# Optimization experiments

Hardware: AMD Instinct MI355X
Metric: run time of the kernel (lower is better)

## Reference

```python
import jax, jax.numpy as jnp
import numpy as np

N = 1024   # nnodes
H = 8      # attention heads
C = 32     # gnn_repr_size (per head)
HC = H * C # 256
E = 65536  # num edges
ER = 32    # edge_repr_size
F = 3      # feat_emb_size
NUM_STOPS = 512


def setup_inputs() -> dict:
    key = jax.random.key(0)
    ks = jax.random.split(key, 24)
    g = lambda i, shape, s: jax.random.normal(ks[i], shape, dtype=jnp.float32) * s
    return {
        "dist": jax.random.uniform(ks[0], (N, N), dtype=jnp.float32),
        "stops": jax.random.randint(ks[1], (NUM_STOPS,), 0, N),
        "weekday": 3,
        "vehicles": 5,
        "markov": jax.random.uniform(ks[2], (N, N), dtype=jnp.float32),
        "demand": jax.random.uniform(ks[3], (N, 1), dtype=jnp.float32),
        "capacity": 10,
        "edge_index": jax.random.randint(ks[4], (2, E), 0, N),
        # GATConv layer 1 (in=1, out=H*C, edge_dim=1)
        "W1": g(5, (1, HC), 1.0), "We1": g(6, (1, HC), 1.0),
        "a_src1": g(7, (H, C), 0.1), "a_dst1": g(8, (H, C), 0.1), "a_edge1": g(9, (H, C), 0.1),
        "b1": jnp.zeros((HC,), jnp.float32),
        # GATConv layer 2 (in=H*C, out=H*C)
        "W2": g(10, (HC, HC), 0.0625), "We2": g(11, (1, HC), 1.0),
        "a_src2": g(12, (H, C), 0.1), "a_dst2": g(13, (H, C), 0.1), "a_edge2": g(14, (H, C), 0.1),
        "b2": jnp.zeros((HC,), jnp.float32),
        # edge summarizer Linear(2*HC, ER)
        "Wes": g(15, (2 * HC, ER), 0.0442), "bes": jnp.zeros((ER,), jnp.float32),
        # scalar embeddings
        "emb_weekday": g(16, (7, F), 0.1), "emb_capacity": g(17, (26, F), 0.1), "emb_vehicle": g(18, (15, F), 0.1),
        # combiner MLP: Linear(N*ER + 3N + 3F, N), Linear(N, N)
        "Wc1": g(19, (N * ER + 3 * N + 3 * F, N), 0.0053), "bc1": jnp.zeros((N,), jnp.float32),
        "Wc2": g(20, (N, N), 0.03125), "bc2": jnp.zeros((N,), jnp.float32),
    }


def _gat(x, src, dst, edge_attr, W, We, a_src, a_dst, a_edge, b):
    """PyG GATConv (concat heads, eval mode so attention dropout is identity)."""
    h = (x @ W).reshape(-1, H, C)                   # [N, H, C]
    e = (edge_attr @ We).reshape(-1, H, C)          # [E, H, C]
    alpha = (h * a_src).sum(-1)[src] + (h * a_dst).sum(-1)[dst] + (e * a_edge).sum(-1)  # [E, H]
    alpha = jax.nn.leaky_relu(alpha, 0.2)
    # segment softmax over destination nodes
    m = jax.ops.segment_max(alpha, dst, num_segments=N)
    m = jnp.where(jnp.isfinite(m), m, 0.0)
    ex = jnp.exp(alpha - m[dst])
    denom = jax.ops.segment_sum(ex, dst, num_segments=N)
    coef = ex / (denom[dst] + 1e-16)                # [E, H]
    out = jax.ops.segment_sum(h[src] * coef[:, :, None], dst, num_segments=N)  # [N, H, C]
    return out.reshape(-1, HC) + b


def reference(dist, stops, weekday, vehicles, markov, demand, capacity, edge_index,
              W1, We1, a_src1, a_dst1, a_edge1, b1,
              W2, We2, a_src2, a_dst2, a_edge2, b2,
              Wes, bes, emb_weekday, emb_capacity, emb_vehicle,
              Wc1, bc1, Wc2, bc2):
    src, dst = edge_index[0], edge_index[1]
    dist = (dist - dist.min()) / (dist.max() - dist.min())
    edge_attr = markov[src, dst][:, None]           # [E, 1]
    x = _gat(demand, src, dst, edge_attr, W1, We1, a_src1, a_dst1, a_edge1, b1)
    x = jax.nn.relu(x)
    x = _gat(x, src, dst, edge_attr, W2, We2, a_src2, a_dst2, a_edge2, b2)
    x = jax.nn.relu(x)                              # [N, HC]
    # edge_summarizer(cat(x_i, x_j)) decomposed: x_i @ Wes_top + x_j @ Wes_bot + bes
    ea = x @ Wes[:HC]                               # [N, ER]
    eb = x @ Wes[HC:]                               # [N, ER]
    edge_repr = (ea[:, None, :] + eb[None, :, :] + bes).reshape(N, N * ER)
    wf = jnp.broadcast_to(emb_weekday[weekday][None, :], (N, F))
    cf = jnp.broadcast_to(emb_capacity[capacity][None, :], (N, F))
    vf = jnp.broadcast_to(emb_vehicle[vehicles][None, :], (N, F))
    sf = jnp.zeros((N,), jnp.float32).at[stops].set(1.0)
    sf = jnp.broadcast_to(sf[None, :], (N, N))
    combined = jnp.concatenate([edge_repr, dist, markov, wf, cf, vf, sf], axis=1)
    out = jax.nn.relu(combined @ Wc1 + bc1) @ Wc2 + bc2  # [N, N]
    return out
```

## Files before the change

### kernel.cpp

```cpp
#include <hip/hip_runtime.h>

#define NN 1024
#define NE 65536

typedef short v8s __attribute__((ext_vector_type(8)));
typedef float v4f __attribute__((ext_vector_type(4)));

constexpr size_t OF_SCAL = 0;
constexpr size_t OF_MMP  = 64;
constexpr size_t OF_DEG  = 1088;
constexpr size_t OF_OFF  = 2112;
constexpr size_t OF_CUR  = 3200;
constexpr size_t OF_EIDX = 4224;
constexpr size_t OF_MARK = 69760;
constexpr size_t OF_T1   = 135296;
constexpr size_t OF_X1   = 143488;
constexpr size_t OF_H2   = 405632;
constexpr size_t OF_S2S  = 667776;
constexpr size_t OF_S2D  = 675968;
constexpr size_t OF_MAX2 = 684160;
constexpr size_t OF_DEN2 = 692352;
constexpr size_t OF_EX2  = 700544;
constexpr size_t OF_X2   = 1224832;
constexpr size_t OF_BCAT = 1486976;
constexpr size_t OF_EAB  = 1503360;
constexpr size_t OF_WVEC = 1568896;
constexpr size_t OF_SRP  = 1604800;
constexpr size_t OF_C0P  = 3701952;
constexpr size_t OF_SR   = 3775680;
constexpr size_t OF_BASE = 3808448;
constexpr size_t OF_AH   = 3809472;
constexpr size_t OF_AL   = 4874432;
constexpr size_t OF_BTH  = 5939392;
constexpr size_t OF_BTL  = 7004352;
constexpr size_t OF_HH   = 8069312;
constexpr size_t OF_HL   = 8593600;
constexpr size_t OF_W2TH = 9117888;
constexpr size_t OF_W2TL = 9642176;
constexpr size_t OF_P0   = 10166464;

__device__ inline unsigned short f2bf(float x){
  unsigned u = __float_as_uint(x);
  unsigned r = u + 0x7fffu + ((u>>16)&1u);
  return (unsigned short)(r>>16);
}
__device__ inline float bf2f(unsigned short h){
  return __uint_as_float(((unsigned)h)<<16);
}

__global__ void k_zero(int* deg){
  int i = blockIdx.x*256 + threadIdx.x;
  if (i < NN) deg[i] = 0;
}

__global__ void k_mm1(const float* __restrict__ dist, float* mnP, float* mxP){
  __shared__ float smn[256], smx[256];
  int tid = threadIdx.x;
  float mn = 1e30f, mx = -1e30f;
  for (int i = blockIdx.x*256 + tid; i < NN*NN; i += gridDim.x*256){
    float v = dist[i]; mn = fminf(mn, v); mx = fmaxf(mx, v);
  }
  smn[tid]=mn; smx[tid]=mx; __syncthreads();
  for (int s=128; s>0; s>>=1){
    if (tid<s){ smn[tid]=fminf(smn[tid],smn[tid+s]); smx[tid]=fmaxf(smx[tid],smx[tid+s]); }
    __syncthreads();
  }
  if (tid==0){ mnP[blockIdx.x]=smn[0]; mxP[blockIdx.x]=smx[0]; }
}

__global__ void k_mm2(const float* mnP, const float* mxP, float* scal){
  __shared__ float smn[512], smx[512];
  int tid = threadIdx.x;
  smn[tid]=mnP[tid]; smx[tid]=mxP[tid]; __syncthreads();
  for (int s=256; s>0; s>>=1){
    if (tid<s){ smn[tid]=fminf(smn[tid],smn[tid+s]); smx[tid]=fmaxf(smx[tid],smx[tid+s]); }
    __syncthreads();
  }
  if (tid==0){ scal[0]=smn[0]; scal[1]=1.0f/(smx[0]-smn[0]); }
}

__global__ void k_prep(const float* W1, const float* We1, const float* as1, const float* ad1,
                       const float* ae1, const float* We2, const float* ae2, float* scal){
  int t = threadIdx.x;
  if (t < 8){
    float s=0.f, d=0.f, e=0.f, e2=0.f;
    for (int c=0;c<32;c++){
      int i = t*32+c;
      s += W1[i]*as1[i]; d += W1[i]*ad1[i]; e += We1[i]*ae1[i]; e2 += We2[i]*ae2[i];
    }
    scal[16+t]=s; scal[24+t]=d; scal[32+t]=e; scal[40+t]=e2;
  }
}

__global__ void k_edges(const int* __restrict__ ei, const float* __restrict__ markov,
                        float* __restrict__ mark, int* __restrict__ deg){
  int e = blockIdx.x*256 + threadIdx.x;
  if (e >= NE) return;
  int s = ei[e], d = ei[NE+e];
  mark[e] = markov[(size_t)s*NN + d];
  atomicAdd(&deg[d], 1);
}

__global__ void k_scan(const int* deg, int* off, int* cur){
  __shared__ int tmp[NN];
  int t = threadIdx.x;
  tmp[t] = deg[t]; __syncthreads();
  for (int s=1; s<NN; s<<=1){
    int v = (t>=s) ? tmp[t-s] : 0;
    __syncthreads();
    tmp[t] += v;
    __syncthreads();
  }
  int ex = (t==0) ? 0 : tmp[t-1];
  off[t]=ex; cur[t]=ex;
  if (t==NN-1) off[NN]=tmp[NN-1];
}

__global__ void k_fill(const int* __restrict__ ei, int* __restrict__ cur, int* __restrict__ eidxl){
  int e = blockIdx.x*256 + threadIdx.x;
  if (e >= NE) return;
  int d = ei[NE+e];
  int p = atomicAdd(&cur[d], 1);
  eidxl[p] = e;
}

__global__ __launch_bounds__(64) void k_gat1(const int* __restrict__ ei, const int* __restrict__ eidxl,
    const int* __restrict__ off, const float* __restrict__ mark, const float* __restrict__ demand,
    const float* __restrict__ scal, float* __restrict__ t1){
  int n = blockIdx.x, lane = threadIdx.x;
  int o0 = off[n], o1 = off[n+1];
  float dn = demand[n];
  float cs[8], cd[8], ce[8], mx[8];
  #pragma unroll
  for (int h=0;h<8;h++){ cs[h]=scal[16+h]; cd[h]=scal[24+h]; ce[h]=scal[32+h]; mx[h]=-1e30f; }
  for (int i=o0+lane; i<o1; i+=64){
    int e = eidxl[i]; float ds = demand[ei[e]]; float me = mark[e];
    #pragma unroll
    for (int h=0;h<8;h++){
      float a = ds*cs[h] + dn*cd[h] + me*ce[h];
      a = a < 0.f ? 0.2f*a : a;
      mx[h] = fmaxf(mx[h], a);
    }
  }
  #pragma unroll
  for (int s=32; s>0; s>>=1){
    #pragma unroll
    for (int h=0;h<8;h++) mx[h] = fmaxf(mx[h], __shfl_xor(mx[h], s));
  }
  float se[8], sd_[8];
  #pragma unroll
  for (int h=0;h<8;h++){ se[h]=0.f; sd_[h]=0.f; }
  for (int i=o0+lane; i<o1; i+=64){
    int e = eidxl[i]; float ds = demand[ei[e]]; float me = mark[e];
    #pragma unroll
    for (int h=0;h<8;h++){
      float a = ds*cs[h] + dn*cd[h] + me*ce[h];
      a = a < 0.f ? 0.2f*a : a;
      float ex = expf(a - mx[h]);
      se[h] += ex; sd_[h] += ex*ds;
    }
  }
  #pragma unroll
  for (int s=32; s>0; s>>=1){
    #pragma unroll
    for (int h=0;h<8;h++){ se[h] += __shfl_xor(se[h], s); sd_[h] += __shfl_xor(sd_[h], s); }
  }
  if (lane==0){
    #pragma unroll
    for (int h=0;h<8;h++) t1[n*8+h] = sd_[h] / (se[h] + 1e-16f);
  }
}

__global__ void k_x1(const float* __restrict__ t1, const float* __restrict__ W1,
                     const float* __restrict__ b1, float* __restrict__ x1){
  int n = blockIdx.x, hc = threadIdx.x, h = hc >> 5;
  x1[(size_t)n*256 + hc] = fmaxf(t1[n*8+h]*W1[hc] + b1[hc], 0.f);
}

__global__ __launch_bounds__(256) void gemm64(const float* __restrict__ A, int lda,
    const float* __restrict__ B, int ldb, float* __restrict__ C, int ldc, int K,
    const float* __restrict__ bias, int dorelu){
  __shared__ float As[16][68];
  __shared__ float Bs[16][68];
  int tid = threadIdx.x;
  int tx = tid & 15, ty = tid >> 4;
  int row0 = ty*4, col0 = tx*4;
  int gm = blockIdx.y*64, gn = blockIdx.x*64;
  float acc[4][4] = {};
  for (int k0 = 0; k0 < K; k0 += 16){
    #pragma unroll
    for (int q=0;q<4;q++){
      int idx = tid*4+q; int i = idx>>4, kk = idx&15;
      As[kk][i] = A[(size_t)(gm+i)*lda + k0 + kk];
    }
    #pragma unroll
    for (int q=0;q<4;q++){
      int idx = tid*4+q; int kk = idx>>6, j = idx&63;
      Bs[kk][j] = B[(size_t)(k0+kk)*ldb + gn + j];
    }
    __syncthreads();
    #pragma unroll
    for (int kk=0;kk<16;kk++){
      float a0=As[kk][row0+0], a1=As[kk][row0+1], a2=As[kk][row0+2], a3=As[kk][row0+3];
      float b0=Bs[kk][col0+0], b1=Bs[kk][col0+1], b2=Bs[kk][col0+2], b3=Bs[kk][col0+3];
      acc[0][0]+=a0*b0; acc[0][1]+=a0*b1; acc[0][2]+=a0*b2; acc[0][3]+=a0*b3;
      acc[1][0]+=a1*b0; acc[1][1]+=a1*b1; acc[1][2]+=a1*b2; acc[1][3]+=a1*b3;
      acc[2][0]+=a2*b0; acc[2][1]+=a2*b1; acc[2][2]+=a2*b2; acc[2][3]+=a2*b3;
      acc[3][0]+=a3*b0; acc[3][1]+=a3*b1; acc[3][2]+=a3*b2; acc[3][3]+=a3*b3;
    }
    __syncthreads();
  }
  #pragma unroll
  for (int i=0;i<4;i++){
    #pragma unroll
    for (int j=0;j<4;j++){
      int cc = gn + col0 + j;
      float v = acc[i][j];
      if (bias) v += bias[cc];
      if (dorelu) v = fmaxf(v, 0.f);
      C[(size_t)(gm+row0+i)*ldc + cc] = v;
    }
  }
}

__global__ void k_s2(const float* __restrict__ h2, const float* __restrict__ as2,
                     const float* __restrict__ ad2, float* __restrict__ s2s, float* __restrict__ s2d){
  int idx = blockIdx.x*256 + threadIdx.x;
  if (idx >= NN*8) return;
  int n = idx >> 3, h = idx & 7;
  float ss = 0.f, sd = 0.f;
  for (int c=0;c<32;c++){
    float v = h2[(size_t)n*256 + h*32 + c];
    ss += v*as2[h*32+c]; sd += v*ad2[h*32+c];
  }
  s2s[idx]=ss; s2d[idx]=sd;
}

__global__ __launch_bounds__(64) void k_gat2max(const int* __restrict__ ei, const int* __restrict__ eidxl,
    const int* __restrict__ off, const float* __restrict__ mark, const float* __restrict__ s2s,
    const float* __restrict__ s2d, const float* __restrict__ scal,
    float* __restrict__ mx2, float* __restrict__ den){
  int n = blockIdx.x, lane = threadIdx.x;
  int o0 = off[n], o1 = off[n+1];
  float ce[8], sdn[8], mx[8];
  #pragma unroll
  for (int h=0;h<8;h++){ ce[h]=scal[40+h]; sdn[h]=s2d[n*8+h]; mx[h]=-1e30f; }
  for (int i=o0+lane; i<o1; i+=64){
    int e = eidxl[i]; int s = ei[e]; float me = mark[e];
    #pragma unroll
    for (int h=0;h<8;h++){
      float a = s2s[s*8+h] + sdn[h] + me*ce[h];
      a = a < 0.f ? 0.2f*a : a;
      mx[h] = fmaxf(mx[h], a);
    }
  }
  #pragma unroll
  for (int sft=32; sft>0; sft>>=1){
    #pragma unroll
    for (int h=0;h<8;h++) mx[h] = fmaxf(mx[h], __shfl_xor(mx[h], sft));
  }
  float se[8];
  #pragma unroll
  for (int h=0;h<8;h++) se[h]=0.f;
  for (int i=o0+lane; i<o1; i+=64){
    int e = eidxl[i]; int s = ei[e]; float me = mark[e];
    #pragma unroll
    for (int h=0;h<8;h++){
      float a = s2s[s*8+h] + sdn[h] + me*ce[h];
      a = a < 0.f ? 0.2f*a : a;
      se[h] += expf(a - mx[h]);
    }
  }
  #pragma unroll
  for (int sft=32; sft>0; sft>>=1){
    #pragma unroll
    for (int h=0;h<8;h++) se[h] += __shfl_xor(se[h], sft);
  }
  if (lane==0){
    #pragma unroll
    for (int h=0;h<8;h++){ mx2[n*8+h] = (o1>o0) ? mx[h] : 0.f; den[n*8+h] = se[h]; }
  }
}

__global__ void k_ex2(const int* __restrict__ ei, const float* __restrict__ mark,
                      const float* __restrict__ s2s, const float* __restrict__ s2d,
                      const float* __restrict__ mx2, const float* __restrict__ scal,
                      float* __restrict__ ex2){
  int e = blockIdx.x*256 + threadIdx.x;
  if (e >= NE) return;
  int s = ei[e], d = ei[NE+e];
  float me = mark[e];
  #pragma unroll
  for (int h=0;h<8;h++){
    float a = s2s[s*8+h] + s2d[d*8+h] + me*scal[40+h];
    a = a < 0.f ? 0.2f*a : a;
    ex2[(size_t)e*8+h] = expf(a - mx2[d*8+h]);
  }
}

__global__ __launch_bounds__(256) void k_agg2(const int* __restrict__ ei, const int* __restrict__ eidxl,
    const int* __restrict__ off, const float* __restrict__ ex2, const float* __restrict__ den,
    const float* __restrict__ h2, const float* __restrict__ b2, float* __restrict__ x2){
  __shared__ int eL[64], sL[64];
  int n = blockIdx.x, tid = threadIdx.x, h = tid >> 5;
  int o0 = off[n], o1 = off[n+1];
  float inv = 1.0f/(den[n*8+h] + 1e-16f);
  float acc = 0.f;
  for (int b = o0; b < o1; b += 64){
    int len = min(64, o1 - b);
    __syncthreads();
    if (tid < len){ int e = eidxl[b+tid]; eL[tid]=e; sL[tid]=ei[e]; }
    __syncthreads();
    for (int j=0;j<len;j++){
      acc += ex2[(size_t)eL[j]*8 + h] * h2[(size_t)sL[j]*256 + tid];
    }
  }
  x2[(size_t)n*256 + tid] = fmaxf(acc*inv + b2[tid], 0.f);
}

__global__ void k_bcat(const float* __restrict__ Wes, float* __restrict__ Bcat){
  int idx = blockIdx.x*256 + threadIdx.x;
  if (idx >= 256*64) return;
  int k = idx >> 6, r = idx & 63;
  Bcat[idx] = (r < 32) ? Wes[(size_t)k*32 + r] : Wes[(size_t)(256+k)*32 + (r-32)];
}

__global__ void k_wvec(const float* __restrict__ eab, const float* __restrict__ bes,
                       const float* __restrict__ ew, const float* __restrict__ ec, const float* __restrict__ ev,
                       const int* __restrict__ wd, const int* __restrict__ cap, const int* __restrict__ veh,
                       float* __restrict__ wvec){
  int m = blockIdx.x*256 + threadIdx.x;
  if (m >= 35849) return;
  float v;
  if (m < 32768){ int j = m >> 5, r = m & 31; v = eab[(size_t)j*64 + 32 + r] + bes[r]; }
  else if (m < 34816) v = 0.f;
  else if (m < 34819) v = ew[wd[0]*3 + (m-34816)];
  else if (m < 34822) v = ec[cap[0]*3 + (m-34819)];
  else if (m < 34825) v = ev[veh[0]*3 + (m-34822)];
  else v = 0.f;
  wvec[m] = v;
}

__global__ void k_stops(const int* __restrict__ stops, float* __restrict__ wvec){
  wvec[34825 + stops[threadIdx.x]] = 1.0f;
}

__global__ __launch_bounds__(256) void k_src0(const float* __restrict__ Wc1, const float* __restrict__ wvec,
                                              float* __restrict__ srP, float* __restrict__ c0P){
  __shared__ float c0s[256*4];
  int t = threadIdx.x;
  int kg = t & 31;
  int rg = t >> 5;
  int col = blockIdx.x*128 + kg*4;
  int chunk = blockIdx.y;
  int m0 = chunk*512;
  float sr[4][4];
  #pragma unroll
  for (int u=0;u<4;u++){ sr[u][0]=0.f; sr[u][1]=0.f; sr[u][2]=0.f; sr[u][3]=0.f; }
  float c0a[4] = {0.f,0.f,0.f,0.f};
  for (int jj=0; jj<16; ++jj){
    int rbase = m0 + jj*32 + rg*4;
    #pragma unroll
    for (int u=0;u<4;u++){
      int m = rbase + u;
      float4 w = make_float4(0.f,0.f,0.f,0.f);
      float wv = 0.f;
      if (m < 35849){
        w = *reinterpret_cast<const float4*>(&Wc1[(size_t)m*1024 + col]);
        wv = wvec[m];
      }
      c0a[0] += wv*w.x; c0a[1] += wv*w.y; c0a[2] += wv*w.z; c0a[3] += wv*w.w;
      if (chunk < 64){
        sr[u][0] += w.x; sr[u][1] += w.y; sr[u][2] += w.z; sr[u][3] += w.w;
      }
    }
  }
  if (chunk < 64){
    #pragma unroll
    for (int u=0;u<4;u++){
      int r = rg*4 + u;
      float4 v = make_float4(sr[u][0], sr[u][1], sr[u][2], sr[u][3]);
      *reinterpret_cast<float4*>(&srP[(size_t)(chunk*32 + r)*1024 + col]) = v;
    }
  }
  c0s[t*4+0]=c0a[0]; c0s[t*4+1]=c0a[1]; c0s[t*4+2]=c0a[2]; c0s[t*4+3]=c0a[3];
  __syncthreads();
  if (t < 32){
    float s0=0.f,s1=0.f,s2=0.f,s3=0.f;
    #pragma unroll
    for (int q=0;q<8;q++){
      int b = (t + q*32)*4;
      s0 += c0s[b+0]; s1 += c0s[b+1]; s2 += c0s[b+2]; s3 += c0s[b+3];
    }
    float4 v = make_float4(s0,s1,s2,s3);
    *reinterpret_cast<float4*>(&c0P[(size_t)chunk*1024 + blockIdx.x*128 + t*4]) = v;
  }
}

__global__ void k_stage2(const float* __restrict__ srP, const float* __restrict__ c0P,
                         const float* __restrict__ bc1, float* __restrict__ Sr, float* __restrict__ base){
  int idx = blockIdx.x*256 + threadIdx.x;
  if (idx < 8192){
    int r = idx >> 8, k4 = idx & 255;
    float s0=0.f,s1=0.f,s2=0.f,s3=0.f;
    for (int c=0;c<64;c++){
      float4 v = *reinterpret_cast<const float4*>(&srP[(size_t)(c*32 + r)*1024 + k4*4]);
      s0+=v.x; s1+=v.y; s2+=v.z; s3+=v.w;
    }
    float4 o = make_float4(s0,s1,s2,s3);
    *reinterpret_cast<float4*>(&Sr[(size_t)r*1024 + k4*4]) = o;
  } else if (idx < 8448){
    int k4 = idx - 8192;
    float4 b = *reinterpret_cast<const float4*>(&bc1[k4*4]);
    float s0=b.x, s1=b.y, s2=b.z, s3=b.w;
    for (int c=0;c<71;c++){
      float4 v = *reinterpret_cast<const float4*>(&c0P[(size_t)c*1024 + k4*4]);
      s0+=v.x; s1+=v.y; s2+=v.z; s3+=v.w;
    }
    float4 o = make_float4(s0,s1,s2,s3);
    *reinterpret_cast<float4*>(&base[k4*4]) = o;
  }
}

__global__ void k_cvtA(const float* __restrict__ dist, const float* __restrict__ markov,
                       const float* __restrict__ eab, const float* __restrict__ scal,
                       unsigned short* __restrict__ Ah, unsigned short* __restrict__ Al){
  int k = blockIdx.x*256 + threadIdx.x;
  int i = blockIdx.y;
  if (k >= 2080) return;
  float mn = scal[0], inv = scal[1];
  float v;
  if (k < 1024) v = (dist[(size_t)i*1024 + k] - mn)*inv;
  else if (k < 2048) v = markov[(size_t)i*1024 + (k-1024)];
  else v = eab[(size_t)i*64 + (k-2048)];
  unsigned short h = f2bf(v);
  Ah[(size_t)i*2080 + k] = h;
  Al[(size_t)i*2080 + k] = f2bf(v - bf2f(h));
}

__global__ void k_cvtT(const float* __restrict__ src, const float* __restrict__ src2, int k2,
                       int ldt, unsigned short* __restrict__ Th, unsigned short* __restrict__ Tl){
  __shared__ unsigned short shh[32][65], shl[32][65];
  int t = threadIdx.x;
  int k0 = blockIdx.x*32, n0 = blockIdx.y*64;
  #pragma unroll
  for (int q=0;q<8;q++){
    int idx = t + q*256;
    int kl = idx >> 6, nl = idx & 63;
    int k = k0 + kl;
    float v = (k < k2) ? src[(size_t)k*1024 + n0 + nl] : src2[(size_t)(k-k2)*1024 + n0 + nl];
    unsigned short h = f2bf(v);
    shh[kl][nl] = h;
    shl[kl][nl] = f2bf(v - bf2f(h));
  }
  __syncthreads();
  #pragma unroll
  for (int q=0;q<8;q++){
    int idx = t + q*256;
    int nl = idx >> 5, kl = idx & 31;
    Th[(size_t)(n0+nl)*ldt + k0 + kl] = shh[kl][nl];
    Tl[(size_t)(n0+nl)*ldt + k0 + kl] = shl[kl][nl];
  }
}

__global__ __launch_bounds__(256) void k_mfma128(
    const unsigned short* __restrict__ Ah, const unsigned short* __restrict__ Al, int lda,
    const unsigned short* __restrict__ Bth, const unsigned short* __restrict__ Btl, int ldb,
    float* __restrict__ Cp, int kSteps, int kTot){
  __shared__ __align__(16) unsigned short Ash[128*32], Asl[128*32], Bsh[128*32], Bsl[128*32];
  int t = threadIdx.x;
  int wave = t >> 6, lane = t & 63;
  int wr = wave >> 1, wc = wave & 1;
  int gm = blockIdx.y*128, gn = blockIdx.x*128;
  float* plane = Cp + ((size_t)blockIdx.z << 20);
  int ks0 = blockIdx.z * kSteps;
  int ks1 = ks0 + kSteps; if (ks1 > kTot) ks1 = kTot;

  int kq = lane >> 4;
  int l15 = lane & 15;

  int r0s = t >> 2,        s0s = t & 3;
  int r1s = (t+256) >> 2,  s1s = t & 3;

  v4f acc[4][4];
  #pragma unroll
  for (int i=0;i<4;i++)
    #pragma unroll
    for (int j=0;j<4;j++) acc[i][j] = (v4f){0.f,0.f,0.f,0.f};

  for (int ks = ks0; ks < ks1; ++ks){
    int kb = ks*32;
    const size_t a0 = (size_t)(gm+r0s)*lda + kb + s0s*8;
    const size_t a1 = (size_t)(gm+r1s)*lda + kb + s1s*8;
    const size_t b0 = (size_t)(gn+r0s)*ldb + kb + s0s*8;
    const size_t b1 = (size_t)(gn+r1s)*ldb + kb + s1s*8;
    v8s gah0 = *(const v8s*)(Ah + a0), gah1 = *(const v8s*)(Ah + a1);
    v8s gal0 = *(const v8s*)(Al + a0), gal1 = *(const v8s*)(Al + a1);
    v8s gbh0 = *(const v8s*)(Bth + b0), gbh1 = *(const v8s*)(Bth + b1);
    v8s gbl0 = *(const v8s*)(Btl + b0), gbl1 = *(const v8s*)(Btl + b1);
    __syncthreads();
    int w0 = r0s*32 + ((s0s ^ ((r0s>>1)&3))*8);
    int w1 = r1s*32 + ((s1s ^ ((r1s>>1)&3))*8);
    *(v8s*)(Ash + w0) = gah0;  *(v8s*)(Ash + w1) = gah1;
    *(v8s*)(Asl + w0) = gal0;  *(v8s*)(Asl + w1) = gal1;
    *(v8s*)(Bsh + w0) = gbh0;  *(v8s*)(Bsh + w1) = gbh1;
    *(v8s*)(Bsl + w0) = gbl0;  *(v8s*)(Bsl + w1) = gbl1;
    __syncthreads();
    v8s fbh[4], fbl[4];
    #pragma unroll
    for (int fj=0; fj<4; fj++){
      int cb = wc*64 + fj*16 + l15;
      int boff = cb*32 + ((kq ^ ((cb>>1)&3))*8);
      fbh[fj] = *(v8s*)(Bsh + boff);
      fbl[fj] = *(v8s*)(Bsl + boff);
    }
    #pragma unroll
    for (int fi=0; fi<4; fi++){
      int ra = wr*64 + fi*16 + l15;
      int aoff = ra*32 + ((kq ^ ((ra>>1)&3))*8);
      v8s fah = *(v8s*)(Ash + aoff);
      v8s fal = *(v8s*)(Asl + aoff);
      #pragma unroll
      for (int fj=0; fj<4; fj++){
        acc[fi][fj] = __builtin_amdgcn_mfma_f32_16x16x32_bf16(fah, fbh[fj], acc[fi][fj], 0, 0, 0);
        acc[fi][fj] = __builtin_amdgcn_mfma_f32_16x16x32_bf16(fah, fbl[fj], acc[fi][fj], 0, 0, 0);
        acc[fi][fj] = __builtin_amdgcn_mfma_f32_16x16x32_bf16(fal, fbh[fj], acc[fi][fj], 0, 0, 0);
      }
    }
  }
  int row0 = gm + wr*64 + (lane>>4)*4;
  int col0 = gn + wc*64 + l15;
  #pragma unroll
  for (int fi=0; fi<4; fi++)
    #pragma unroll
    for (int fj=0; fj<4; fj++)
      #pragma unroll
      for (int r=0; r<4; r++)
        plane[(size_t)(row0 + fi*16 + r)*1024 + col0 + fj*16] = acc[fi][fj][r];
}

__global__ void k_fin_hidden(const float* __restrict__ P, const float* __restrict__ base,
                             unsigned short* __restrict__ Hh, unsigned short* __restrict__ Hl){
  int idx = blockIdx.x*256 + threadIdx.x;
  float4 v0 = *reinterpret_cast<const float4*>(P + (size_t)idx*4);
  float4 v1 = *reinterpret_cast<const float4*>(P + (1u<<20) + (size_t)idx*4);
  float4 v2 = *reinterpret_cast<const float4*>(P + (2u<<20) + (size_t)idx*4);
  float4 v3 = *reinterpret_cast<const float4*>(P + (3u<<20) + (size_t)idx*4);
  float4 b  = *reinterpret_cast<const float4*>(base + ((idx & 255)*4));
  float v[4] = { v0.x+v1.x+v2.x+v3.x+b.x, v0.y+v1.y+v2.y+v3.y+b.y,
                 v0.z+v1.z+v2.z+v3.z+b.z, v0.w+v1.w+v2.w+v3.w+b.w };
  unsigned short hh[4], hl[4];
  #pragma unroll
  for (int q=0;q<4;q++){
    float x = fmaxf(v[q], 0.f);
    hh[q] = f2bf(x);
    hl[q] = f2bf(x - bf2f(hh[q]));
  }
  *reinterpret_cast<uint2*>(Hh + (size_t)idx*4) = *reinterpret_cast<uint2*>(hh);
  *reinterpret_cast<uint2*>(Hl + (size_t)idx*4) = *reinterpret_cast<uint2*>(hl);
}

__global__ void k_fin_out(const float* __restrict__ P, const float* __restrict__ bc2,
                          float* __restrict__ out){
  int idx = blockIdx.x*256 + threadIdx.x;
  float4 v0 = *reinterpret_cast<const float4*>(P + (size_t)idx*4);
  float4 v1 = *reinterpret_cast<const float4*>(P + (1u<<20) + (size_t)idx*4);
  float4 v2 = *reinterpret_cast<const float4*>(P + (2u<<20) + (size_t)idx*4);
  float4 v3 = *reinterpret_cast<const float4*>(P + (3u<<20) + (size_t)idx*4);
  float4 b  = *reinterpret_cast<const float4*>(bc2 + ((idx & 255)*4));
  float4 o = make_float4(v0.x+v1.x+v2.x+v3.x+b.x, v0.y+v1.y+v2.y+v3.y+b.y,
                         v0.z+v1.z+v2.z+v3.z+b.z, v0.w+v1.w+v2.w+v3.w+b.w);
  *reinterpret_cast<float4*>(out + (size_t)idx*4) = o;
}

extern "C" void kernel_launch(void* const* d_in, const int* in_sizes, int n_in,
                              void* d_out, int out_size, void* d_ws, size_t ws_size,
                              hipStream_t stream){
  const float* dist     = (const float*)d_in[0];
  const int*   stops    = (const int*)  d_in[1];
  const int*   weekday  = (const int*)  d_in[2];
  const int*   vehicles = (const int*)  d_in[3];
  const float* markov   = (const float*)d_in[4];
  const float* demand   = (const float*)d_in[5];
  const int*   capacity = (const int*)  d_in[6];
  const int*   ei       = (const int*)  d_in[7];
  const float* W1  = (const float*)d_in[8];
  const float* We1 = (const float*)d_in[9];
  const float* as1 = (const float*)d_in[10];
  const float* ad1 = (const float*)d_in[11];
  const float* ae1 = (const float*)d_in[12];
  const float* b1  = (const float*)d_in[13];
  const float* W2  = (const float*)d_in[14];
  const float* We2 = (const float*)d_in[15];
  const float* as2 = (const float*)d_in[16];
  const float* ad2 = (const float*)d_in[17];
  const float* ae2 = (const float*)d_in[18];
  const float* b2  = (const float*)d_in[19];
  const float* Wes = (const float*)d_in[20];
  const float* bes = (const float*)d_in[21];
  const float* ew  = (const float*)d_in[22];
  const float* ec  = (const float*)d_in[23];
  const float* ev  = (const float*)d_in[24];
  const float* Wc1 = (const float*)d_in[25];
  const float* bc1 = (const float*)d_in[26];
  const float* Wc2 = (const float*)d_in[27];
  const float* bc2 = (const float*)d_in[28];

  float* W    = (float*)d_ws;
  float* scal = W + OF_SCAL;
  float* mmP  = W + OF_MMP;
  int*   deg  = (int*)(W + OF_DEG);
  int*   off  = (int*)(W + OF_OFF);
  int*   cur  = (int*)(W + OF_CUR);
  int*   eidxl= (int*)(W + OF_EIDX);
  float* mark = W + OF_MARK;
  float* t1   = W + OF_T1;
  float* x1   = W + OF_X1;
  float* h2   = W + OF_H2;
  float* s2s  = W + OF_S2S;
  float* s2d  = W + OF_S2D;
  float* mx2  = W + OF_MAX2;
  float* den2 = W + OF_DEN2;
  float* ex2  = W + OF_EX2;
  float* x2   = W + OF_X2;
  float* Bcat = W + OF_BCAT;
  float* eab  = W + OF_EAB;
  float* wvec = W + OF_WVEC;
  float* srP  = W + OF_SRP;
  float* c0P  = W + OF_C0P;
  float* Sr   = W + OF_SR;
  float* base = W + OF_BASE;
  unsigned short* Ah   = (unsigned short*)(W + OF_AH);
  unsigned short* Al   = (unsigned short*)(W + OF_AL);
  unsigned short* Bth  = (unsigned short*)(W + OF_BTH);
  unsigned short* Btl  = (unsigned short*)(W + OF_BTL);
  unsigned short* Hh   = (unsigned short*)(W + OF_HH);
  unsigned short* Hl   = (unsigned short*)(W + OF_HL);
  unsigned short* W2th = (unsigned short*)(W + OF_W2TH);
  unsigned short* W2tl = (unsigned short*)(W + OF_W2TL);
  float* P0   = W + OF_P0;
  float* out  = (float*)d_out;

  k_zero<<<dim3(4), dim3(256), 0, stream>>>(deg);
  k_mm1 <<<dim3(512), dim3(256), 0, stream>>>(dist, mmP, mmP+512);
  k_mm2 <<<dim3(1), dim3(512), 0, stream>>>(mmP, mmP+512, scal);
  k_prep<<<dim3(1), dim3(64), 0, stream>>>(W1, We1, as1, ad1, ae1, We2, ae2, scal);
  k_edges<<<dim3(256), dim3(256), 0, stream>>>(ei, markov, mark, deg);
  k_scan<<<dim3(1), dim3(1024), 0, stream>>>(deg, off, cur);
  k_fill<<<dim3(256), dim3(256), 0, stream>>>(ei, cur, eidxl);
  k_gat1<<<dim3(1024), dim3(64), 0, stream>>>(ei, eidxl, off, mark, demand, scal, t1);
  k_x1  <<<dim3(1024), dim3(256), 0, stream>>>(t1, W1, b1, x1);
  gemm64<<<dim3(4,16), dim3(256), 0, stream>>>(x1, 256, W2, 256, h2, 256, 256, (const float*)nullptr, 0);
  k_s2  <<<dim3(32), dim3(256), 0, stream>>>(h2, as2, ad2, s2s, s2d);
  k_gat2max<<<dim3(1024), dim3(64), 0, stream>>>(ei, eidxl, off, mark, s2s, s2d, scal, mx2, den2);
  k_ex2 <<<dim3(256), dim3(256), 0, stream>>>(ei, mark, s2s, s2d, mx2, scal, ex2);
  k_agg2<<<dim3(1024), dim3(256), 0, stream>>>(ei, eidxl, off, ex2, den2, h2, b2, x2);
  k_bcat<<<dim3(64), dim3(256), 0, stream>>>(Wes, Bcat);
  gemm64<<<dim3(1,16), dim3(256), 0, stream>>>(x2, 256, Bcat, 64, eab, 64, 256, (const float*)nullptr, 0);
  k_wvec<<<dim3(141), dim3(256), 0, stream>>>(eab, bes, ew, ec, ev, weekday, capacity, vehicles, wvec);
  k_stops<<<dim3(1), dim3(512), 0, stream>>>(stops, wvec);
  k_src0<<<dim3(8,71), dim3(256), 0, stream>>>(Wc1, wvec, srP, c0P);
  k_stage2<<<dim3(33), dim3(256), 0, stream>>>(srP, c0P, bc1, Sr, base);
  k_cvtA<<<dim3(9,1024), dim3(256), 0, stream>>>(dist, markov, eab, scal, Ah, Al);
  k_cvtT<<<dim3(65,16), dim3(256), 0, stream>>>(Wc1 + (size_t)32768*1024, Sr, 2048, 2080, Bth, Btl);
  k_cvtT<<<dim3(32,16), dim3(256), 0, stream>>>(Wc2, Wc2, 1<<30, 1024, W2th, W2tl);
  k_mfma128<<<dim3(8,8,4), dim3(256), 0, stream>>>(Ah, Al, 2080, Bth, Btl, 2080, P0, 17, 65);
  k_fin_hidden<<<dim3(1024), dim3(256), 0, stream>>>(P0, base, Hh, Hl);
  k_mfma128<<<dim3(8,8,4), dim3(256), 0, stream>>>(Hh, Hl, 1024, W2th, W2tl, 1024, P0, 8, 32);
  k_fin_out<<<dim3(1024), dim3(256), 0, stream>>>(P0, bc2, out);
}
```

Before: 224.8 us.

## Fuse small prep kernels, move GAT2 GEMM to split-bf16 MFMA, double split-K

Merges several tiny setup kernels (zeroing, min/max finish, scalar prep, Bcat, embedding/stop vector writes) into fewer launches. It fuses GAT1 with the x1 projection, which now emits hi/lo bf16 pairs for an MFMA GEMM that replaces the fp32 gemm64 for W2. It also folds the ex2 computation into the max/denominator pass, and stages attention coefficients in shared memory for aggregation. Split-K for the two large combiner GEMMs rises from 4 to 8 partial planes. These changes aim to cut launch overhead and improve GEMM occupancy, at the cost of more partial-sum traffic in the finalize kernels.

```diff
diff --git a/kernel.cpp b/kernel.cpp
--- a/kernel.cpp
+++ b/kernel.cpp
@@ -13,31 +13,32 @@
 constexpr size_t OF_CUR  = 3200;
 constexpr size_t OF_EIDX = 4224;
 constexpr size_t OF_MARK = 69760;
-constexpr size_t OF_T1   = 135296;
-constexpr size_t OF_X1   = 143488;
-constexpr size_t OF_H2   = 405632;
-constexpr size_t OF_S2S  = 667776;
-constexpr size_t OF_S2D  = 675968;
-constexpr size_t OF_MAX2 = 684160;
-constexpr size_t OF_DEN2 = 692352;
-constexpr size_t OF_EX2  = 700544;
-constexpr size_t OF_X2   = 1224832;
-constexpr size_t OF_BCAT = 1486976;
-constexpr size_t OF_EAB  = 1503360;
-constexpr size_t OF_WVEC = 1568896;
-constexpr size_t OF_SRP  = 1604800;
-constexpr size_t OF_C0P  = 3701952;
-constexpr size_t OF_SR   = 3775680;
-constexpr size_t OF_BASE = 3808448;
-constexpr size_t OF_AH   = 3809472;
-constexpr size_t OF_AL   = 4874432;
-constexpr size_t OF_BTH  = 5939392;
-constexpr size_t OF_BTL  = 7004352;
-constexpr size_t OF_HH   = 8069312;
-constexpr size_t OF_HL   = 8593600;
-constexpr size_t OF_W2TH = 9117888;
-constexpr size_t OF_W2TL = 9642176;
-constexpr size_t OF_P0   = 10166464;
+constexpr size_t OF_X1H  = 135296;
+constexpr size_t OF_X1L  = 266368;
+constexpr size_t OF_H2   = 397440;
+constexpr size_t OF_S2S  = 659584;
+constexpr size_t OF_S2D  = 667776;
+constexpr size_t OF_DEN2 = 675968;
+constexpr size_t OF_EX2  = 684160;
+constexpr size_t OF_X2   = 1208448;
+constexpr size_t OF_BCAT = 1470592;
+constexpr size_t OF_EAB  = 1486976;
+constexpr size_t OF_WVEC = 1552512;
+constexpr size_t OF_SRP  = 1588608;
+constexpr size_t OF_C0P  = 3685760;
+constexpr size_t OF_SR   = 3759488;
+constexpr size_t OF_BASE = 3792256;
+constexpr size_t OF_AH   = 3793280;
+constexpr size_t OF_AL   = 4858240;
+constexpr size_t OF_BTH  = 5923200;
+constexpr size_t OF_BTL  = 6988160;
+constexpr size_t OF_HH   = 8053120;
+constexpr size_t OF_HL   = 8577408;
+constexpr size_t OF_W2TH = 9101696;
+constexpr size_t OF_W2TL = 9134464;
+constexpr size_t OF_WC2TH= 9167232;
+constexpr size_t OF_WC2TL= 9691520;
+constexpr size_t OF_P0   = 10215808;
 
 __device__ inline unsigned short f2bf(float x){
   unsigned u = __float_as_uint(x);
@@ -48,14 +49,10 @@
   return __uint_as_float(((unsigned)h)<<16);
 }
 
-__global__ void k_zero(int* deg){
-  int i = blockIdx.x*256 + threadIdx.x;
-  if (i < NN) deg[i] = 0;
-}
-
-__global__ void k_mm1(const float* __restrict__ dist, float* mnP, float* mxP){
+__global__ void k_mm1(const float* __restrict__ dist, float* mnP, float* mxP, int* __restrict__ deg){
   __shared__ float smn[256], smx[256];
   int tid = threadIdx.x;
+  if (blockIdx.x < 4) deg[blockIdx.x*256 + tid] = 0;
   float mn = 1e30f, mx = -1e30f;
   for (int i = blockIdx.x*256 + tid; i < NN*NN; i += gridDim.x*256){
     float v = dist[i]; mn = fminf(mn, v); mx = fmaxf(mx, v);
@@ -68,27 +65,44 @@
   if (tid==0){ mnP[blockIdx.x]=smn[0]; mxP[blockIdx.x]=smx[0]; }
 }
 
-__global__ void k_mm2(const float* mnP, const float* mxP, float* scal){
-  __shared__ float smn[512], smx[512];
-  int tid = threadIdx.x;
-  smn[tid]=mnP[tid]; smx[tid]=mxP[tid]; __syncthreads();
-  for (int s=256; s>0; s>>=1){
-    if (tid<s){ smn[tid]=fminf(smn[tid],smn[tid+s]); smx[tid]=fmaxf(smx[tid],smx[tid+s]); }
-    __syncthreads();
-  }
-  if (tid==0){ scal[0]=smn[0]; scal[1]=1.0f/(smx[0]-smn[0]); }
-}
-
-__global__ void k_prep(const float* W1, const float* We1, const float* as1, const float* ad1,
-                       const float* ae1, const float* We2, const float* ae2, float* scal){
-  int t = threadIdx.x;
-  if (t < 8){
-    float s=0.f, d=0.f, e=0.f, e2=0.f;
-    for (int c=0;c<32;c++){
-      int i = t*32+c;
-      s += W1[i]*as1[i]; d += W1[i]*ad1[i]; e += We1[i]*ae1[i]; e2 += We2[i]*ae2[i];
-    }
-    scal[16+t]=s; scal[24+t]=d; scal[32+t]=e; scal[40+t]=e2;
+__global__ __launch_bounds__(512) void k_misc(const float* mnP, const float* mxP, float* scal,
+    const float* W1, const float* We1, const float* as1, const float* ad1, const float* ae1,
+    const float* We2, const float* ae2,
+    const float* ew, const float* ec, const float* ev,
+    const int* wd, const int* cap, const int* veh, const int* stops, float* wvec,
+    const float* Wes, float* Bcat){
+  int b = blockIdx.x, t = threadIdx.x;
+  if (b == 0){
+    __shared__ float smn[512], smx[512];
+    smn[t]=mnP[t]; smx[t]=mxP[t]; __syncthreads();
+    for (int s=256; s>0; s>>=1){
+      if (t<s){ smn[t]=fminf(smn[t],smn[t+s]); smx[t]=fmaxf(smx[t],smx[t+s]); }
+      __syncthreads();
+    }
+    if (t==0){ scal[0]=smn[0]; scal[1]=1.0f/(smx[0]-smn[0]); }
+  } else if (b == 1){
+    if (t < 8){
+      float s=0.f, d=0.f, e=0.f, e2=0.f;
+      for (int c=0;c<32;c++){
+        int i = t*32+c;
+        s += W1[i]*as1[i]; d += W1[i]*ad1[i]; e += We1[i]*ae1[i]; e2 += We2[i]*ae2[i];
+      }
+      scal[16+t]=s; scal[24+t]=d; scal[32+t]=e; scal[40+t]=e2;
+    }
+  } else if (b == 2){
+    for (int m = 32768 + t; m < 35904; m += 512){
+      float v = 0.f;
+      if (m >= 34816 && m < 34819) v = ew[wd[0]*3 + (m-34816)];
+      else if (m >= 34819 && m < 34822) v = ec[cap[0]*3 + (m-34819)];
+      else if (m >= 34822 && m < 34825) v = ev[veh[0]*3 + (m-34822)];
+      wvec[m] = v;
+    }
+    __syncthreads();
+    wvec[34825 + stops[t]] = 1.0f;
+  } else {
+    int idx = (b-3)*512 + t;
+    int k = idx >> 6, r = idx & 63;
+    Bcat[idx] = (r < 32) ? Wes[(size_t)k*32 + r] : Wes[(size_t)(256+k)*32 + (r-32)];
   }
 }
 
@@ -124,9 +138,10 @@
   eidxl[p] = e;
 }
 
-__global__ __launch_bounds__(64) void k_gat1(const int* __restrict__ ei, const int* __restrict__ eidxl,
+__global__ __launch_bounds__(64) void k_gat1x1(const int* __restrict__ ei, const int* __restrict__ eidxl,
     const int* __restrict__ off, const float* __restrict__ mark, const float* __restrict__ demand,
-    const float* __restrict__ scal, float* __restrict__ t1){
+    const float* __restrict__ scal, const float* __restrict__ W1, const float* __restrict__ b1,
+    unsigned short* __restrict__ X1h, unsigned short* __restrict__ X1l){
   int n = blockIdx.x, lane = threadIdx.x;
   int o0 = off[n], o1 = off[n+1];
   float dn = demand[n];
@@ -165,16 +180,17 @@
     #pragma unroll
     for (int h=0;h<8;h++){ se[h] += __shfl_xor(se[h], s); sd_[h] += __shfl_xor(sd_[h], s); }
   }
-  if (lane==0){
-    #pragma unroll
-    for (int h=0;h<8;h++) t1[n*8+h] = sd_[h] / (se[h] + 1e-16f);
-  }
-}
-
-__global__ void k_x1(const float* __restrict__ t1, const float* __restrict__ W1,
-                     const float* __restrict__ b1, float* __restrict__ x1){
-  int n = blockIdx.x, hc = threadIdx.x, h = hc >> 5;
-  x1[(size_t)n*256 + hc] = fmaxf(t1[n*8+h]*W1[hc] + b1[hc], 0.f);
+  float t1v[8];
+  #pragma unroll
+  for (int h=0;h<8;h++) t1v[h] = sd_[h] / (se[h] + 1e-16f);
+  #pragma unroll
+  for (int q=0;q<4;q++){
+    int hc = lane + q*64; int h = hc >> 5;
+    float v = fmaxf(t1v[h]*W1[hc] + b1[hc], 0.f);
+    unsigned short hh = f2bf(v);
+    X1h[(size_t)n*256 + hc] = hh;
+    X1l[(size_t)n*256 + hc] = f2bf(v - bf2f(hh));
+  }
 }
 
 __global__ __launch_bounds__(256) void gemm64(const float* __restrict__ A, int lda,
@@ -236,10 +252,10 @@
   s2s[idx]=ss; s2d[idx]=sd;
 }
 
-__global__ __launch_bounds__(64) void k_gat2max(const int* __restrict__ ei, const int* __restrict__ eidxl,
+__global__ __launch_bounds__(64) void k_gat2maxex(const int* __restrict__ ei, const int* __restrict__ eidxl,
     const int* __restrict__ off, const float* __restrict__ mark, const float* __restrict__ s2s,
     const float* __restrict__ s2d, const float* __restrict__ scal,
-    float* __restrict__ mx2, float* __restrict__ den){
+    float* __restrict__ den, float* __restrict__ ex2){
   int n = blockIdx.x, lane = threadIdx.x;
   int o0 = off[n], o1 = off[n+1];
   float ce[8], sdn[8], mx[8];
@@ -264,12 +280,16 @@
   for (int h=0;h<8;h++) se[h]=0.f;
   for (int i=o0+lane; i<o1; i+=64){
     int e = eidxl[i]; int s = ei[e]; float me = mark[e];
+    float exv[8];
     #pragma unroll
     for (int h=0;h<8;h++){
       float a = s2s[s*8+h] + sdn[h] + me*ce[h];
       a = a < 0.f ? 0.2f*a : a;
-      se[h] += expf(a - mx[h]);
-    }
+      exv[h] = expf(a - mx[h]);
+      se[h] += exv[h];
+    }
+    #pragma unroll
+    for (int h=0;h<8;h++) ex2[(size_t)e*8+h] = exv[h];
   }
   #pragma unroll
   for (int sft=32; sft>0; sft>>=1){
@@ -278,23 +298,7 @@
   }
   if (lane==0){
     #pragma unroll
-    for (int h=0;h<8;h++){ mx2[n*8+h] = (o1>o0) ? mx[h] : 0.f; den[n*8+h] = se[h]; }
-  }
-}
-
-__global__ void k_ex2(const int* __restrict__ ei, const float* __restrict__ mark,
-                      const float* __restrict__ s2s, const float* __restrict__ s2d,
-                      const float* __restrict__ mx2, const float* __restrict__ scal,
-                      float* __restrict__ ex2){
-  int e = blockIdx.x*256 + threadIdx.x;
-  if (e >= NE) return;
-  int s = ei[e], d = ei[NE+e];
-  float me = mark[e];
-  #pragma unroll
-  for (int h=0;h<8;h++){
-    float a = s2s[s*8+h] + s2d[d*8+h] + me*scal[40+h];
-    a = a < 0.f ? 0.2f*a : a;
-    ex2[(size_t)e*8+h] = expf(a - mx2[d*8+h]);
+    for (int h=0;h<8;h++) den[n*8+h] = se[h];
   }
 }
 
@@ -302,6 +306,7 @@
     const int* __restrict__ off, const float* __restrict__ ex2, const float* __restrict__ den,
     const float* __restrict__ h2, const float* __restrict__ b2, float* __restrict__ x2){
   __shared__ int eL[64], sL[64];
+  __shared__ float cf[64*8];
   int n = blockIdx.x, tid = threadIdx.x, h = tid >> 5;
   int o0 = off[n], o1 = off[n+1];
   float inv = 1.0f/(den[n*8+h] + 1e-16f);
@@ -311,38 +316,21 @@
     __syncthreads();
     if (tid < len){ int e = eidxl[b+tid]; eL[tid]=e; sL[tid]=ei[e]; }
     __syncthreads();
+    for (int idx = tid; idx < len*8; idx += 256)
+      cf[idx] = ex2[(size_t)eL[idx>>3]*8 + (idx&7)];
+    __syncthreads();
     for (int j=0;j<len;j++){
-      acc += ex2[(size_t)eL[j]*8 + h] * h2[(size_t)sL[j]*256 + tid];
+      acc += cf[j*8 + h] * h2[(size_t)sL[j]*256 + tid];
     }
   }
   x2[(size_t)n*256 + tid] = fmaxf(acc*inv + b2[tid], 0.f);
 }
 
-__global__ void k_bcat(const float* __restrict__ Wes, float* __restrict__ Bcat){
-  int idx = blockIdx.x*256 + threadIdx.x;
-  if (idx >= 256*64) return;
-  int k = idx >> 6, r = idx & 63;
-  Bcat[idx] = (r < 32) ? Wes[(size_t)k*32 + r] : Wes[(size_t)(256+k)*32 + (r-32)];
-}
-
 __global__ void k_wvec(const float* __restrict__ eab, const float* __restrict__ bes,
-                       const float* __restrict__ ew, const float* __restrict__ ec, const float* __restrict__ ev,
-                       const int* __restrict__ wd, const int* __restrict__ cap, const int* __restrict__ veh,
                        float* __restrict__ wvec){
   int m = blockIdx.x*256 + threadIdx.x;
-  if (m >= 35849) return;
-  float v;
-  if (m < 32768){ int j = m >> 5, r = m & 31; v = eab[(size_t)j*64 + 32 + r] + bes[r]; }
-  else if (m < 34816) v = 0.f;
-  else if (m < 34819) v = ew[wd[0]*3 + (m-34816)];
-  else if (m < 34822) v = ec[cap[0]*3 + (m-34819)];
-  else if (m < 34825) v = ev[veh[0]*3 + (m-34822)];
-  else v = 0.f;
-  wvec[m] = v;
-}
-
-__global__ void k_stops(const int* __restrict__ stops, float* __restrict__ wvec){
-  wvec[34825 + stops[threadIdx.x]] = 1.0f;
+  int j = m >> 5, r = m & 31;
+  wvec[m] = eab[(size_t)j*64 + 32 + r] + bes[r];
 }
 
 __global__ __launch_bounds__(256) void k_src0(const float* __restrict__ Wc1, const float* __restrict__ wvec,
@@ -439,7 +427,7 @@
 }
 
 __global__ void k_cvtT(const float* __restrict__ src, const float* __restrict__ src2, int k2,
-                       int ldt, unsigned short* __restrict__ Th, unsigned short* __restrict__ Tl){
+                       int lds, int ldt, unsigned short* __restrict__ Th, unsigned short* __restrict__ Tl){
   __shared__ unsigned short shh[32][65], shl[32][65];
   int t = threadIdx.x;
   int k0 = blockIdx.x*32, n0 = blockIdx.y*64;
@@ -448,7 +436,7 @@
     int idx = t + q*256;
     int kl = idx >> 6, nl = idx & 63;
     int k = k0 + kl;
-    float v = (k < k2) ? src[(size_t)k*1024 + n0 + nl] : src2[(size_t)(k-k2)*1024 + n0 + nl];
+    float v = (k < k2) ? src[(size_t)k*lds + n0 + nl] : src2[(size_t)(k-k2)*lds + n0 + nl];
     unsigned short h = f2bf(v);
     shh[kl][nl] = h;
     shl[kl][nl] = f2bf(v - bf2f(h));
@@ -466,7 +454,7 @@
 __global__ __launch_bounds__(256) void k_mfma128(
     const unsigned short* __restrict__ Ah, const unsigned short* __restrict__ Al, int lda,
     const unsigned short* __restrict__ Bth, const unsigned short* __restrict__ Btl, int ldb,
-    float* __restrict__ Cp, int kSteps, int kTot){
+    float* __restrict__ Cp, int ldc, int kSteps, int kTot){
   __shared__ __align__(16) unsigned short Ash[128*32], Asl[128*32], Bsh[128*32], Bsl[128*32];
   int t = threadIdx.x;
   int wave = t >> 6, lane = t & 63;
@@ -478,7 +466,6 @@
 
   int kq = lane >> 4;
   int l15 = lane & 15;
-
   int r0s = t >> 2,        s0s = t & 3;
   int r1s = (t+256) >> 2,  s1s = t & 3;
 
@@ -536,23 +523,31 @@
     for (int fj=0; fj<4; fj++)
       #pragma unroll
       for (int r=0; r<4; r++)
-        plane[(size_t)(row0 + fi*16 + r)*1024 + col0 + fj*16] = acc[fi][fj][r];
+        plane[(size_t)(row0 + fi*16 + r)*ldc + col0 + fj*16] = acc[fi][fj][r];
+}
+
+__global__ void k_fin2(const float* __restrict__ P, float* __restrict__ h2){
+  int idx = blockIdx.x*256 + threadIdx.x;
+  float4 a = *reinterpret_cast<const float4*>(P + (size_t)idx*4);
+  float4 b = *reinterpret_cast<const float4*>(P + (1u<<20) + (size_t)idx*4);
+  float4 o = make_float4(a.x+b.x, a.y+b.y, a.z+b.z, a.w+b.w);
+  *reinterpret_cast<float4*>(h2 + (size_t)idx*4) = o;
 }
 
 __global__ void k_fin_hidden(const float* __restrict__ P, const float* __restrict__ base,
                              unsigned short* __restrict__ Hh, unsigned short* __restrict__ Hl){
   int idx = blockIdx.x*256 + threadIdx.x;
-  float4 v0 = *reinterpret_cast<const float4*>(P + (size_t)idx*4);
-  float4 v1 = *reinterpret_cast<const float4*>(P + (1u<<20) + (size_t)idx*4);
-  float4 v2 = *reinterpret_cast<const float4*>(P + (2u<<20) + (size_t)idx*4);
-  float4 v3 = *reinterpret_cast<const float4*>(P + (3u<<20) + (size_t)idx*4);
-  float4 b  = *reinterpret_cast<const float4*>(base + ((idx & 255)*4));
-  float v[4] = { v0.x+v1.x+v2.x+v3.x+b.x, v0.y+v1.y+v2.y+v3.y+b.y,
-                 v0.z+v1.z+v2.z+v3.z+b.z, v0.w+v1.w+v2.w+v3.w+b.w };
+  float4 s = *reinterpret_cast<const float4*>(base + ((idx & 255)*4));
+  #pragma unroll
+  for (int p=0;p<8;p++){
+    float4 v = *reinterpret_cast<const float4*>(P + ((size_t)p<<20) + (size_t)idx*4);
+    s.x+=v.x; s.y+=v.y; s.z+=v.z; s.w+=v.w;
+  }
+  float vv[4] = {s.x, s.y, s.z, s.w};
   unsigned short hh[4], hl[4];
   #pragma unroll
   for (int q=0;q<4;q++){
-    float x = fmaxf(v[q], 0.f);
+    float x = fmaxf(vv[q], 0.f);
     hh[q] = f2bf(x);
     hl[q] = f2bf(x - bf2f(hh[q]));
   }
@@ -563,14 +558,13 @@
 __global__ void k_fin_out(const float* __restrict__ P, const float* __restrict__ bc2,
                           float* __restrict__ out){
   int idx = blockIdx.x*256 + threadIdx.x;
-  float4 v0 = *reinterpret_cast<const float4*>(P + (size_t)idx*4);
-  float4 v1 = *reinterpret_cast<const float4*>(P + (1u<<20) + (size_t)idx*4);
-  float4 v2 = *reinterpret_cast<const float4*>(P + (2u<<20) + (size_t)idx*4);
-  float4 v3 = *reinterpret_cast<const float4*>(P + (3u<<20) + (size_t)idx*4);
-  float4 b  = *reinterpret_cast<const float4*>(bc2 + ((idx & 255)*4));
-  float4 o = make_float4(v0.x+v1.x+v2.x+v3.x+b.x, v0.y+v1.y+v2.y+v3.y+b.y,
-                         v0.z+v1.z+v2.z+v3.z+b.z, v0.w+v1.w+v2.w+v3.w+b.w);
-  *reinterpret_cast<float4*>(out + (size_t)idx*4) = o;
+  float4 s = *reinterpret_cast<const float4*>(bc2 + ((idx & 255)*4));
+  #pragma unroll
+  for (int p=0;p<8;p++){
+    float4 v = *reinterpret_cast<const float4*>(P + ((size_t)p<<20) + (size_t)idx*4);
+    s.x+=v.x; s.y+=v.y; s.z+=v.z; s.w+=v.w;
+  }
+  *reinterpret_cast<float4*>(out + (size_t)idx*4) = s;
 }
 
 extern "C" void kernel_launch(void* const* d_in, const int* in_sizes, int n_in,
@@ -614,12 +608,11 @@
   int*   cur  = (int*)(W + OF_CUR);
   int*   eidxl= (int*)(W + OF_EIDX);
   float* mark = W + OF_MARK;
-  float* t1   = W + OF_T1;
-  float* x1   = W + OF_X1;
+  unsigned short* X1h = (unsigned short*)(W + OF_X1H);
+  unsigned short* X1l = (unsigned short*)(W + OF_X1L);
   float* h2   = W + OF_H2;
   float* s2s  = W + OF_S2S;
   float* s2d  = W + OF_S2D;
-  float* mx2  = W + OF_MAX2;
   float* den2 = W + OF_DEN2;
   float* ex2  = W + OF_EX2;
   float* x2   = W + OF_X2;
@@ -630,42 +623,41 @@
   float* c0P  = W + OF_C0P;
   float* Sr   = W + OF_SR;
   float* base = W + OF_BASE;
-  unsigned short* Ah   = (unsigned short*)(W + OF_AH);
-  unsigned short* Al   = (unsigned short*)(W + OF_AL);
-  unsigned short* Bth  = (unsigned short*)(W + OF_BTH);
-  unsigned short* Btl  = (unsigned short*)(W + OF_BTL);
-  unsigned short* Hh   = (unsigned short*)(W + OF_HH);
-  unsigned short* Hl   = (unsigned short*)(W + OF_HL);
-  unsigned short* W2th = (unsigned short*)(W + OF_W2TH);
-  unsigned short* W2tl = (unsigned short*)(W + OF_W2TL);
+  unsigned short* Ah    = (unsigned short*)(W + OF_AH);
+  unsigned short* Al    = (unsigned short*)(W + OF_AL);
+  unsigned short* Bth   = (unsigned short*)(W + OF_BTH);
+  unsigned short* Btl   = (unsigned short*)(W + OF_BTL);
+  unsigned short* Hh    = (unsigned short*)(W + OF_HH);
+  unsigned short* Hl    = (unsigned short*)(W + OF_HL);
+  unsigned short* W2th  = (unsigned short*)(W + OF_W2TH);
+  unsigned short* W2tl  = (unsigned short*)(W + OF_W2TL);
+  unsigned short* Wc2th = (unsigned short*)(W + OF_WC2TH);
+  unsigned short* Wc2tl = (unsigned short*)(W + OF_WC2TL);
   float* P0   = W + OF_P0;
   float* out  = (float*)d_out;
 
-  k_zero<<<dim3(4), dim3(256), 0, stream>>>(deg);
-  k_mm1 <<<dim3(512), dim3(256), 0, stream>>>(dist, mmP, mmP+512);
-  k_mm2 <<<dim3(1), dim3(512), 0, stream>>>(mmP, mmP+512, scal);
-  k_prep<<<dim3(1), dim3(64), 0, stream>>>(W1, We1, as1, ad1, ae1, We2, ae2, scal);
+  k_mm1 <<<dim3(512), dim3(256), 0, stream>>>(dist, mmP, mmP+512, deg);
+  k_misc<<<dim3(35), dim3(512), 0, stream>>>(mmP, mmP+512, scal, W1, We1, as1, ad1, ae1, We2, ae2,
+                                             ew, ec, ev, weekday, capacity, vehicles, stops, wvec, Wes, Bcat);
+  k_cvtT<<<dim3(8,4), dim3(256), 0, stream>>>(W2, W2, 1<<30, 256, 256, W2th, W2tl);
+  k_cvtT<<<dim3(32,16), dim3(256), 0, stream>>>(Wc2, Wc2, 1<<30, 1024, 1024, Wc2th, Wc2tl);
   k_edges<<<dim3(256), dim3(256), 0, stream>>>(ei, markov, mark, deg);
   k_scan<<<dim3(1), dim3(1024), 0, stream>>>(deg, off, cur);
   k_fill<<<dim3(256), dim3(256), 0, stream>>>(ei, cur, eidxl);
-  k_gat1<<<dim3(1024), dim3(64), 0, stream>>>(ei, eidxl, off, mark, demand, scal, t1);
-  k_x1  <<<dim3(1024), dim3(256), 0, stream>>>(t1, W1, b1, x1);
-  gemm64<<<dim3(4,16), dim3(256), 0, stream>>>(x1, 256, W2, 256, h2, 256, 256, (const float*)nullptr, 0);
+  k_gat1x1<<<dim3(1024), dim3(64), 0, stream>>>(ei, eidxl, off, mark, demand, scal, W1, b1, X1h, X1l);
+  k_mfma128<<<dim3(2,8,2), dim3(256), 0, stream>>>(X1h, X1l, 256, W2th, W2tl, 256, P0, 256, 4, 8);
+  k_fin2<<<dim3(256), dim3(256), 0, stream>>>(P0, h2);
   k_s2  <<<dim3(32), dim3(256), 0, stream>>>(h2, as2, ad2, s2s, s2d);
-  k_gat2max<<<dim3(1024), dim3(64), 0, stream>>>(ei, eidxl, off, mark, s2s, s2d, scal, mx2, den2);
-  k_ex2 <<<dim3(256), dim3(256), 0, stream>>>(ei, mark, s2s, s2d, mx2, scal, ex2);
+  k_gat2maxex<<<dim3(1024), dim3(64), 0, stream>>>(ei, eidxl, off, mark, s2s, s2d, scal, den2, ex2);
   k_agg2<<<dim3(1024), dim3(256), 0, stream>>>(ei, eidxl, off, ex2, den2, h2, b2, x2);
-  k_bcat<<<dim3(64), dim3(256), 0, stream>>>(Wes, Bcat);
   gemm64<<<dim3(1,16), dim3(256), 0, stream>>>(x2, 256, Bcat, 64, eab, 64, 256, (const float*)nullptr, 0);
-  k_wvec<<<dim3(141), dim3(256), 0, stream>>>(eab, bes, ew, ec, ev, weekday, capacity, vehicles, wvec);
-  k_stops<<<dim3(1), dim3(512), 0, stream>>>(stops, wvec);
+  k_wvec<<<dim3(128), dim3(256), 0, stream>>>(eab, bes, wvec);
   k_src0<<<dim3(8,71), dim3(256), 0, stream>>>(Wc1, wvec, srP, c0P);
   k_stage2<<<dim3(33), dim3(256), 0, stream>>>(srP, c0P, bc1, Sr, base);
   k_cvtA<<<dim3(9,1024), dim3(256), 0, stream>>>(dist, markov, eab, scal, Ah, Al);
-  k_cvtT<<<dim3(65,16), dim3(256), 0, stream>>>(Wc1 + (size_t)32768*1024, Sr, 2048, 2080, Bth, Btl);
-  k_cvtT<<<dim3(32,16), dim3(256), 0, stream>>>(Wc2, Wc2, 1<<30, 1024, W2th, W2tl);
-  k_mfma128<<<dim3(8,8,4), dim3(256), 0, stream>>>(Ah, Al, 2080, Bth, Btl, 2080, P0, 17, 65);
+  k_cvtT<<<dim3(65,16), dim3(256), 0, stream>>>(Wc1 + (size_t)32768*1024, Sr, 2048, 1024, 2080, Bth, Btl);
+  k_mfma128<<<dim3(8,8,8), dim3(256), 0, stream>>>(Ah, Al, 2080, Bth, Btl, 2080, P0, 1024, 9, 65);
   k_fin_hidden<<<dim3(1024), dim3(256), 0, stream>>>(P0, base, Hh, Hl);
-  k_mfma128<<<dim3(8,8,4), dim3(256), 0, stream>>>(Hh, Hl, 1024, W2th, W2tl, 1024, P0, 8, 32);
+  k_mfma128<<<dim3(8,8,8), dim3(256), 0, stream>>>(Hh, Hl, 1024, Wc2th, Wc2tl, 1024, P0, 1024, 4, 32);
   k_fin_out<<<dim3(1024), dim3(256), 0, stream>>>(P0, bc2, out);
 }
```

New measurement: 201.0 us. 1.12x faster.
